# Optimization experiments

Measured on AMD Instinct MI355X. Metric: run time of the kernel, lower is better.

## Reference

```python
import math
import jax, jax.numpy as jnp
import numpy as np

N_NODES = 100000
N_EDGES = 1600000
IN_DIM, HID_DIM, OUT_DIM = 8, 64, 112


def _glorot(key, fan_in, fan_out):
    lim = math.sqrt(6.0 / (fan_in + fan_out))
    return jax.random.uniform(key, (fan_in, fan_out), jnp.float32, -lim, lim)


def _layer_params(key, in_d, out_d):
    ks = jax.random.split(key, 8)
    return dict(
        Wq=_glorot(ks[0], in_d, out_d), bq=jnp.zeros((out_d,), jnp.float32),
        Wk=_glorot(ks[1], in_d, out_d), bk=jnp.zeros((out_d,), jnp.float32),
        Wv=_glorot(ks[2], in_d, out_d), bv=jnp.zeros((out_d,), jnp.float32),
        Ws=_glorot(ks[3], in_d, out_d), bs=jnp.zeros((out_d,), jnp.float32),
    )


def setup_inputs() -> dict:
    key = jax.random.key(0)
    kx, ke, k0, k1, k2 = jax.random.split(key, 5)
    inp = {
        'x': jax.random.normal(kx, (N_NODES, IN_DIM), jnp.float32),
        'edge_index': jax.random.randint(ke, (2, N_EDGES), 0, N_NODES, jnp.int64),
    }
    for li, (kk, ind, outd) in enumerate([(k0, IN_DIM, HID_DIM), (k1, HID_DIM, HID_DIM), (k2, HID_DIM, OUT_DIM)]):
        p = _layer_params(kk, ind, outd)
        for name, v in p.items():
            inp[f'{name}{li}'] = v
    return inp


def _transformer_conv(x, src, dst, Wq, bq, Wk, bk, Wv, bv, Ws, bs):
    # heads=1, concat=True, no edge_attr, eval mode (no dropout)
    N = x.shape[0]
    C = Wq.shape[1]
    q = x @ Wq + bq            # [N, C]
    k = x @ Wk + bk
    v = x @ Wv + bv
    # per-edge attention score: <q_dst, k_src> / sqrt(C)
    scores = jnp.sum(q[dst] * k[src], axis=-1) * (1.0 / math.sqrt(C))  # [E]
    # segment softmax over destination neighborhoods (stable)
    m = jax.ops.segment_max(scores, dst, num_segments=N)               # [N]
    e = jnp.exp(scores - m[dst])                                       # [E]
    denom = jax.ops.segment_sum(e, dst, num_segments=N)                # [N]
    alpha = e / denom[dst]                                             # [E]
    # weighted scatter-add of source values to destinations
    out = jax.ops.segment_sum(alpha[:, None] * v[src], dst, num_segments=N)  # [N, C]
    # root/skip connection
    return out + (x @ Ws + bs)


def reference(x, edge_index,
              Wq0, bq0, Wk0, bk0, Wv0, bv0, Ws0, bs0,
              Wq1, bq1, Wk1, bk1, Wv1, bv1, Ws1, bs1,
              Wq2, bq2, Wk2, bk2, Wv2, bv2, Ws2, bs2):
    src, dst = edge_index[0], edge_index[1]
    h = _transformer_conv(x, src, dst, Wq0, bq0, Wk0, bk0, Wv0, bv0, Ws0, bs0)
    h = jax.nn.relu(h)
    h = _transformer_conv(h, src, dst, Wq1, bq1, Wk1, bk1, Wv1, bv1, Ws1, bs1)
    h = jax.nn.relu(h)
    out = _transformer_conv(h, src, dst, Wq2, bq2, Wk2, bk2, Wv2, bv2, Ws2, bs2)
    return out
```

## Files before the change

### kernel.cpp

```cpp
#include <hip/hip_runtime.h>
#include <hip/hip_fp16.h>
#include <math.h>
#include <float.h>

#define NN 100000
#define NE 1600000

#define SCAN_T 256
#define SCAN_E 1024
#define SCAN_NB ((NN + SCAN_E - 1) / SCAN_E)

#define NBUCK ((NN + 255) / 256)
#define EPB   4096
#define NBLK  ((NE + EPB - 1) / EPB)
#define HISTN (NBUCK * NBLK)
#define GS_NB ((HISTN + SCAN_E - 1) / SCAN_E)
#define BCAP  5120

template<int IN, int OUT, int NPT, int NWIN>
__global__ __launch_bounds__(256)
void linear_qkvs(const float* __restrict__ x,
                 const float* __restrict__ Wq, const float* __restrict__ bq,
                 const float* __restrict__ Wk, const float* __restrict__ bk,
                 const float* __restrict__ Wv, const float* __restrict__ bv,
                 const float* __restrict__ Ws, const float* __restrict__ bs,
                 float* __restrict__ q, unsigned short* __restrict__ kv,
                 float* __restrict__ outskip) {
    const int t    = threadIdx.x;
    const int lane = t & 63;
    const int wv   = t >> 6;
    const int wid  = blockIdx.y * 4 + wv;
    const int mat  = wid / NWIN;
    const int win  = wid % NWIN;
    const int c    = win * 64 + lane;
    const bool act = (c < OUT);
    const int cl   = act ? c : (OUT - 1);

    const float* W = (mat == 0) ? Wq : (mat == 1) ? Wk : (mat == 2) ? Wv : Ws;
    const float* B = (mat == 0) ? bq : (mat == 1) ? bk : (mat == 2) ? bv : bs;

    const int node0 = blockIdx.x * NPT;
    const float* xrow = x + (size_t)node0 * IN;

    float acc[NPT];
    float bias = B[cl];
#pragma unroll
    for (int p = 0; p < NPT; ++p) acc[p] = bias;

    for (int i0 = 0; i0 < IN; i0 += 4) {
        float w0 = W[(size_t)(i0 + 0) * OUT + cl];
        float w1 = W[(size_t)(i0 + 1) * OUT + cl];
        float w2 = W[(size_t)(i0 + 2) * OUT + cl];
        float w3 = W[(size_t)(i0 + 3) * OUT + cl];
#pragma unroll
        for (int p = 0; p < NPT; ++p) {
            float4 xv = *(const float4*)(xrow + p * IN + i0);
            acc[p] += xv.x * w0 + xv.y * w1 + xv.z * w2 + xv.w * w3;
        }
    }

    if (mat == 0) {
        if (act) {
#pragma unroll
            for (int p = 0; p < NPT; ++p)
                q[(size_t)(node0 + p) * OUT + c] = acc[p];
        }
    } else if (mat == 3) {
        if (act) {
#pragma unroll
            for (int p = 0; p < NPT; ++p)
                outskip[(size_t)(node0 + p) * OUT + c] = acc[p];
        }
    } else {
        const int base = (mat == 1) ? 0 : OUT;
#pragma unroll
        for (int p = 0; p < NPT; ++p) {
            float other = __shfl_xor(acc[p], 1);
            if (act && !(lane & 1)) {
                unsigned lo  = __half_as_ushort(__float2half_rn(acc[p]));
                unsigned hiu = __half_as_ushort(__float2half_rn(other));
                *(unsigned*)(kv + (size_t)(node0 + p) * (2 * OUT) + base + c)
                    = lo | (hiu << 16);
            }
        }
    }
}

__global__ __launch_bounds__(256)
void bin_count(const int* __restrict__ ei, int* __restrict__ hist) {
    __shared__ int h[NBUCK];
    const int t = threadIdx.x;
    for (int i = t; i < NBUCK; i += 256) h[i] = 0;
    __syncthreads();
    int e0 = blockIdx.x * EPB;
    int e1 = e0 + EPB < NE ? e0 + EPB : NE;
    for (int i = e0 + t; i < e1; i += 256)
        atomicAdd(&h[ei[NE + i] >> 8], 1);
    __syncthreads();
    for (int i = t; i < NBUCK; i += 256)
        hist[(size_t)i * NBLK + blockIdx.x] = h[i];
}

__global__ __launch_bounds__(SCAN_T)
void gscan1(int* __restrict__ a, int* __restrict__ bsums) {
    __shared__ int lds[SCAN_T];
    int t = threadIdx.x;
    int base = blockIdx.x * SCAN_E + t * 4;
    int vals[4];
    int s = 0;
#pragma unroll
    for (int j = 0; j < 4; ++j) {
        int idx = base + j;
        vals[j] = (idx < HISTN) ? a[idx] : 0;
        s += vals[j];
    }
    lds[t] = s;
    __syncthreads();
    for (int off = 1; off < SCAN_T; off <<= 1) {
        int xx = (t >= off) ? lds[t - off] : 0;
        __syncthreads();
        lds[t] += xx;
        __syncthreads();
    }
    int run = (t > 0) ? lds[t - 1] : 0;
    if (t == SCAN_T - 1) bsums[blockIdx.x] = lds[t];
#pragma unroll
    for (int j = 0; j < 4; ++j) {
        int idx = base + j;
        if (idx < HISTN) a[idx] = run;
        run += vals[j];
    }
}

__global__ __launch_bounds__(256)
void gscan2(int* __restrict__ bsums) {
    __shared__ int lds[256];
    int t = threadIdx.x;
    lds[t] = (t < GS_NB) ? bsums[t] : 0;
    __syncthreads();
    for (int off = 1; off < 256; off <<= 1) {
        int xx = (t >= off) ? lds[t - off] : 0;
        __syncthreads();
        lds[t] += xx;
        __syncthreads();
    }
    if (t < GS_NB) bsums[t] = (t > 0) ? lds[t - 1] : 0;
}

__global__ __launch_bounds__(256)
void gscan3(int* __restrict__ a, const int* __restrict__ bsums,
            int* __restrict__ bstart) {
    int i = blockIdx.x * 256 + threadIdx.x;
    if (i < HISTN) {
        int v = a[i] + bsums[i / SCAN_E];
        a[i] = v;
        if (i % NBLK == 0) bstart[i / NBLK] = v;
    }
    if (i == 0) bstart[NBUCK] = NE;
}

__global__ __launch_bounds__(256)
void bin_scatter(const int* __restrict__ ei, const int* __restrict__ hist,
                 unsigned* __restrict__ ebuf) {
    __shared__ int off[NBUCK];
    const int t = threadIdx.x;
    for (int i = t; i < NBUCK; i += 256)
        off[i] = hist[(size_t)i * NBLK + blockIdx.x];
    __syncthreads();
    int e0 = blockIdx.x * EPB;
    int e1 = e0 + EPB < NE ? e0 + EPB : NE;
    for (int i = e0 + t; i < e1; i += 256) {
        int src = ei[i];
        int dst = ei[NE + i];
        int b = dst >> 8;
        int p = atomicAdd(&off[b], 1);
        ebuf[p] = ((unsigned)(dst & 255) << 17) | (unsigned)src;
    }
}

__global__ __launch_bounds__(256)
void bucket_hist(const int* __restrict__ bstart,
                 const unsigned* __restrict__ ebuf,
                 int* __restrict__ counts) {
    __shared__ int h[256];
    const int b = blockIdx.x;
    const int t = threadIdx.x;
    h[t] = 0;
    __syncthreads();
    int beg = bstart[b], end = bstart[b + 1];
    for (int i = beg + t; i < end; i += 256)
        atomicAdd(&h[ebuf[i] >> 17], 1);
    __syncthreads();
    int d = b * 256 + t;
    if (d < NN) counts[d] = h[t];
}

__global__ __launch_bounds__(SCAN_T)
void scan1(const int* __restrict__ counts, int* __restrict__ offsets,
           int* __restrict__ blocksums) {
    __shared__ int lds[SCAN_T];
    int t = threadIdx.x;
    int base = blockIdx.x * SCAN_E + t * 4;
    int vals[4];
    int s = 0;
#pragma unroll
    for (int j = 0; j < 4; ++j) {
        int idx = base + j;
        vals[j] = (idx < NN) ? counts[idx] : 0;
        s += vals[j];
    }
    lds[t] = s;
    __syncthreads();
    for (int off = 1; off < SCAN_T; off <<= 1) {
        int xx = (t >= off) ? lds[t - off] : 0;
        __syncthreads();
        lds[t] += xx;
        __syncthreads();
    }
    int run = (t > 0) ? lds[t - 1] : 0;
    if (t == SCAN_T - 1) blocksums[blockIdx.x] = lds[t];
#pragma unroll
    for (int j = 0; j < 4; ++j) {
        int idx = base + j;
        if (idx < NN) offsets[idx] = run;
        run += vals[j];
    }
}

__global__ __launch_bounds__(128)
void scan2(int* __restrict__ blocksums) {
    __shared__ int lds[128];
    int t = threadIdx.x;
    lds[t] = (t < SCAN_NB) ? blocksums[t] : 0;
    __syncthreads();
    for (int off = 1; off < 128; off <<= 1) {
        int xx = (t >= off) ? lds[t - off] : 0;
        __syncthreads();
        lds[t] += xx;
        __syncthreads();
    }
    if (t < SCAN_NB) blocksums[t] = (t > 0) ? lds[t - 1] : 0;
}

__global__ __launch_bounds__(256)
void scan3(int* __restrict__ offsets, const int* __restrict__ blocksums) {
    int i = blockIdx.x * blockDim.x + threadIdx.x;
    if (i < NN) offsets[i] = offsets[i] + blocksums[i / SCAN_E];
    if (i == 0) offsets[NN] = NE;
}

__global__ __launch_bounds__(256)
void csr_write(const int* __restrict__ bstart,
               const unsigned* __restrict__ ebuf,
               const int* __restrict__ offsets,
               int* __restrict__ sorted_src) {
    __shared__ int h[256];
    __shared__ int pre[256];
    __shared__ int posi[256];
    __shared__ unsigned srt[BCAP];
    const int b = blockIdx.x;
    const int t = threadIdx.x;
    h[t] = 0;
    __syncthreads();
    int beg = bstart[b];
    int cnt = bstart[b + 1] - beg;
    cnt = cnt < BCAP ? cnt : BCAP;
    const unsigned* buf = ebuf + beg;
    for (int i = t; i < cnt; i += 256)
        atomicAdd(&h[buf[i] >> 17], 1);
    __syncthreads();
    int v = h[t];
    pre[t] = v;
    __syncthreads();
    for (int off = 1; off < 256; off <<= 1) {
        int xx = (t >= off) ? pre[t - off] : 0;
        __syncthreads();
        pre[t] += xx;
        __syncthreads();
    }
    posi[t] = pre[t] - v;
    __syncthreads();
    for (int i = t; i < cnt; i += 256) {
        unsigned u = buf[i];
        int dl = u >> 17;
        int p = atomicAdd(&posi[dl], 1);
        srt[p] = u & 0x1FFFFu;
    }
    __syncthreads();
    const int base = offsets[b << 8];
    for (int i = t; i < cnt; i += 256)
        sorted_src[base + i] = (int)srt[i];
}

__device__ __forceinline__ float row16_sum(float x) {
    int y;
    y = __builtin_amdgcn_update_dpp(0, __float_as_int(x), 0x121, 0xF, 0xF, true); x += __int_as_float(y);
    y = __builtin_amdgcn_update_dpp(0, __float_as_int(x), 0x122, 0xF, 0xF, true); x += __int_as_float(y);
    y = __builtin_amdgcn_update_dpp(0, __float_as_int(x), 0x124, 0xF, 0xF, true); x += __int_as_float(y);
    y = __builtin_amdgcn_update_dpp(0, __float_as_int(x), 0x128, 0xF, 0xF, true); x += __int_as_float(y);
    return x;
}

__device__ __forceinline__ float4 h4_to_f4(uint2 w) {
    union { unsigned u; __half2 h; } a, b;
    a.u = w.x; b.u = w.y;
    float2 f0 = __half22float2(a.h);
    float2 f1 = __half22float2(b.h);
    return make_float4(f0.x, f0.y, f1.x, f1.y);
}

template<int C, bool RELU>
__global__ __launch_bounds__(256)
void attn_gather(const int* __restrict__ offsets,
                 const int* __restrict__ sorted_src,
                 const float* __restrict__ q,
                 const unsigned short* __restrict__ kv,
                 float* __restrict__ out, float scale) {
    const int wid  = (int)((blockIdx.x * blockDim.x + threadIdx.x) >> 6);
    const int lane = threadIdx.x & 63;
    if (wid >= NN) return;
    const int grp = lane >> 4;
    const int ch  = (lane & 15) * 4;
    constexpr bool P2 = (C > 64);
    const bool hi = P2 && (ch + 64 < C);

    const int beg = offsets[wid], end = offsets[wid + 1];

    float4 qv0 = *(const float4*)(q + (size_t)wid * C + ch);
    float4 qv1 = make_float4(0.f, 0.f, 0.f, 0.f);
    if (hi) qv1 = *(const float4*)(q + (size_t)wid * C + ch + 64);

    float m = -FLT_MAX, l = 0.f;
    float4 a0 = make_float4(0.f, 0.f, 0.f, 0.f);
    float4 a1 = make_float4(0.f, 0.f, 0.f, 0.f);

    int i = beg + grp;
    uint2 kw0 = make_uint2(0, 0), vw0 = kw0, kw1 = kw0, vw1 = kw0;
    if (i < end) {
        const unsigned short* row = kv + (size_t)sorted_src[i] * (2 * C);
        kw0 = *(const uint2*)(row + ch);
        vw0 = *(const uint2*)(row + C + ch);
        if (hi) {
            kw1 = *(const uint2*)(row + 64 + ch);
            vw1 = *(const uint2*)(row + C + 64 + ch);
        }
    }
    while (i < end) {
        int inext = i + 4;
        uint2 nkw0 = make_uint2(0, 0), nvw0 = nkw0, nkw1 = nkw0, nvw1 = nkw0;
        if (inext < end) {
            const unsigned short* row = kv + (size_t)sorted_src[inext] * (2 * C);
            nkw0 = *(const uint2*)(row + ch);
            nvw0 = *(const uint2*)(row + C + ch);
            if (hi) {
                nkw1 = *(const uint2*)(row + 64 + ch);
                nvw1 = *(const uint2*)(row + C + 64 + ch);
            }
        }
        float4 kf0 = h4_to_f4(kw0);
        float4 vf0 = h4_to_f4(vw0);
        float part = qv0.x * kf0.x + qv0.y * kf0.y + qv0.z * kf0.z + qv0.w * kf0.w;
        float4 kf1, vf1;
        if (P2) {
            kf1 = h4_to_f4(kw1);
            vf1 = h4_to_f4(vw1);
            part += qv1.x * kf1.x + qv1.y * kf1.y + qv1.z * kf1.z + qv1.w * kf1.w;
        }
        float s = row16_sum(part) * scale;
        float mn = fmaxf(m, s);
        float al = __expf(m - mn);
        float w  = __expf(s - mn);
        l = l * al + w;
        a0.x = a0.x * al + w * vf0.x; a0.y = a0.y * al + w * vf0.y;
        a0.z = a0.z * al + w * vf0.z; a0.w = a0.w * al + w * vf0.w;
        if (P2) {
            a1.x = a1.x * al + w * vf1.x; a1.y = a1.y * al + w * vf1.y;
            a1.z = a1.z * al + w * vf1.z; a1.w = a1.w * al + w * vf1.w;
        }
        m = mn;
        kw0 = nkw0; vw0 = nvw0; kw1 = nkw1; vw1 = nvw1;
        i = inext;
    }

#pragma unroll
    for (int d = 16; d <= 32; d <<= 1) {
        float mo = __shfl_xor(m, d);
        float lo = __shfl_xor(l, d);
        float4 ao0, ao1;
        ao0.x = __shfl_xor(a0.x, d); ao0.y = __shfl_xor(a0.y, d);
        ao0.z = __shfl_xor(a0.z, d); ao0.w = __shfl_xor(a0.w, d);
        if (P2) {
            ao1.x = __shfl_xor(a1.x, d); ao1.y = __shfl_xor(a1.y, d);
            ao1.z = __shfl_xor(a1.z, d); ao1.w = __shfl_xor(a1.w, d);
        }
        float mn = fmaxf(m, mo);
        float e1 = (l  > 0.f) ? __expf(m  - mn) : 0.f;
        float e2 = (lo > 0.f) ? __expf(mo - mn) : 0.f;
        l = l * e1 + lo * e2;
        a0.x = a0.x * e1 + ao0.x * e2; a0.y = a0.y * e1 + ao0.y * e2;
        a0.z = a0.z * e1 + ao0.z * e2; a0.w = a0.w * e1 + ao0.w * e2;
        if (P2) {
            a1.x = a1.x * e1 + ao1.x * e2; a1.y = a1.y * e1 + ao1.y * e2;
            a1.z = a1.z * e1 + ao1.z * e2; a1.w = a1.w * e1 + ao1.w * e2;
        }
        m = mn;
    }

    if (lane < 16) {
        float inv = (l > 0.f) ? 1.f / l : 0.f;
        size_t o = (size_t)wid * C + ch;
        float4 sk = *(const float4*)(out + o);
        float4 r;
        r.x = sk.x + a0.x * inv; r.y = sk.y + a0.y * inv;
        r.z = sk.z + a0.z * inv; r.w = sk.w + a0.w * inv;
        if (RELU) {
            r.x = fmaxf(r.x, 0.f); r.y = fmaxf(r.y, 0.f);
            r.z = fmaxf(r.z, 0.f); r.w = fmaxf(r.w, 0.f);
        }
        *(float4*)(out + o) = r;
        if (hi) {
            float4 sk1 = *(const float4*)(out + o + 64);
            float4 r1;
            r1.x = sk1.x + a1.x * inv; r1.y = sk1.y + a1.y * inv;
            r1.z = sk1.z + a1.z * inv; r1.w = sk1.w + a1.w * inv;
            if (RELU) {
                r1.x = fmaxf(r1.x, 0.f); r1.y = fmaxf(r1.y, 0.f);
                r1.z = fmaxf(r1.z, 0.f); r1.w = fmaxf(r1.w, 0.f);
            }
            *(float4*)(out + o + 64) = r1;
        }
    }
}

template<int IN, int OUT, bool RELU>
static void run_layer(const float* xin, const float* const* Wb,
                      const int* offsets, const int* sorted_src,
                      float* q, unsigned short* kv,
                      float* out, hipStream_t stream) {
    constexpr int NPT  = 16;
    constexpr int NWIN = (OUT + 63) / 64;
    dim3 gl(NN / NPT, NWIN);
    linear_qkvs<IN, OUT, NPT, NWIN><<<gl, 256, 0, stream>>>(
        xin, Wb[0], Wb[1], Wb[2], Wb[3], Wb[4], Wb[5], Wb[6], Wb[7],
        q, kv, out);

    float scale = 1.0f / sqrtf((float)OUT);
    attn_gather<OUT, RELU><<<(NN + 3) / 4, 256, 0, stream>>>(
        offsets, sorted_src, q, kv, out, scale);
}

extern "C" void kernel_launch(void* const* d_in, const int* in_sizes, int n_in,
                              void* d_out, int out_size, void* d_ws, size_t ws_size,
                              hipStream_t stream) {
    const float* x  = (const float*)d_in[0];
    const int*   ei = (const int*)d_in[1];
    const float* Wb0[8], *Wb1[8], *Wb2[8];
    for (int i = 0; i < 8; ++i) {
        Wb0[i] = (const float*)d_in[2 + i];
        Wb1[i] = (const float*)d_in[10 + i];
        Wb2[i] = (const float*)d_in[18 + i];
    }
    float* out = (float*)d_out;

    char* ws = (char*)d_ws;
    const size_t CMAX = 112;
    size_t off = 0;
    float*          q  = (float*)(ws + off);          off += (size_t)NN * CMAX * 4;
    unsigned short* kv = (unsigned short*)(ws + off); off += (size_t)NN * 2 * CMAX * 2;
    float* h0          = (float*)(ws + off);          off += (size_t)NN * 64 * 4;
    float* h1          = (float*)(ws + off);          off += (size_t)NN * 64 * 4;
    int*   sorted_src  = (int*)(ws + off);            off += (size_t)NE * 4;
    int*   counts      = (int*)(ws + off);            off += (size_t)NN * 4;
    int*   offsets     = (int*)(ws + off);            off += (size_t)(NN + 1) * 4;
    int*   blocksums   = (int*)(ws + off);            off += (size_t)SCAN_NB * 4;
    int*   hist        = (int*)(ws + off);            off += (size_t)HISTN * 4;
    int*   gsums       = (int*)(ws + off);            off += (size_t)GS_NB * 4;
    int*   bstart      = (int*)(ws + off);            off += (size_t)(NBUCK + 1) * 4;
    unsigned* ebuf     = (unsigned*)(ws + off);       off += (size_t)NE * 4;
    (void)ws_size; (void)in_sizes; (void)n_in; (void)out_size;

    bin_count<<<NBLK, 256, 0, stream>>>(ei, hist);
    gscan1<<<GS_NB, SCAN_T, 0, stream>>>(hist, gsums);
    gscan2<<<1, 256, 0, stream>>>(gsums);
    gscan3<<<(HISTN + 255) / 256, 256, 0, stream>>>(hist, gsums, bstart);
    bin_scatter<<<NBLK, 256, 0, stream>>>(ei, hist, ebuf);
    bucket_hist<<<NBUCK, 256, 0, stream>>>(bstart, ebuf, counts);
    scan1<<<SCAN_NB, SCAN_T, 0, stream>>>(counts, offsets, blocksums);
    scan2<<<1, 128, 0, stream>>>(blocksums);
    scan3<<<(NN + 255) / 256, 256, 0, stream>>>(offsets, blocksums);
    csr_write<<<NBUCK, 256, 0, stream>>>(bstart, ebuf, offsets, sorted_src);

    run_layer<8,  64, true >(x,  Wb0, offsets, sorted_src, q, kv, h0,  stream);
    run_layer<64, 64, true >(h0, Wb1, offsets, sorted_src, q, kv, h1,  stream);
    run_layer<64, 112, false>(h1, Wb2, offsets, sorted_src, q, kv, out, stream);
}
```

Before: 631.2 us.

## Compute QKVS projections with split-bf16 MFMA instead of scalar FP32 FMA

Replaces the scalar FP32 linear kernel with an MFMA-based GEMM that splits both activations and weights into bf16 hi/lo parts and accumulates three 16x16x32 products to keep close to FP32 accuracy. A new prep kernel repacks the weights into the MFMA fragment layout once per call, placed in the workspace after the edge buffer once CSR building is done. The goal is to cut the per-layer projection cost, paid for with extra conversion work, three MFMAs per tile and a small precision loss from dropping the lo*lo term.

```diff
diff --git a/kernel.cpp b/kernel.cpp
--- a/kernel.cpp
+++ b/kernel.cpp
@@ -2,6 +2,7 @@
 #include <hip/hip_fp16.h>
 #include <math.h>
 #include <float.h>
+#include <stdint.h>
 
 #define NN 100000
 #define NE 1600000
@@ -17,70 +18,153 @@
 #define GS_NB ((HISTN + SCAN_E - 1) / SCAN_E)
 #define BCAP  5120
 
-template<int IN, int OUT, int NPT, int NWIN>
-__global__ __launch_bounds__(256)
-void linear_qkvs(const float* __restrict__ x,
-                 const float* __restrict__ Wq, const float* __restrict__ bq,
-                 const float* __restrict__ Wk, const float* __restrict__ bk,
-                 const float* __restrict__ Wv, const float* __restrict__ bv,
-                 const float* __restrict__ Ws, const float* __restrict__ bs,
-                 float* __restrict__ q, unsigned short* __restrict__ kv,
-                 float* __restrict__ outskip) {
+typedef __attribute__((ext_vector_type(8))) short short8v;
+typedef __attribute__((ext_vector_type(4))) float float4v;
+
+__device__ __forceinline__ unsigned short f32_to_bf16_rne(float f) {
+    unsigned u = __float_as_uint(f);
+    u += 0x7FFFu + ((u >> 16) & 1u);
+    return (unsigned short)(u >> 16);
+}
+__device__ __forceinline__ float bf16_to_f32(unsigned short h) {
+    return __uint_as_float(((unsigned)h) << 16);
+}
+
+template<int K, int OUT>
+__global__ __launch_bounds__(256)
+void prep_w(const float* __restrict__ Wq, const float* __restrict__ Wk,
+            const float* __restrict__ Wv, const float* __restrict__ Ws,
+            unsigned short* __restrict__ wsp) {
+    constexpr int NKS  = (K + 31) / 32;
+    constexpr int OUTT = 4 * OUT;
+    constexpr int NCT  = OUTT / 16;
+    int idx = blockIdx.x * 256 + threadIdx.x;
+    if (idx >= NCT * NKS * 512) return;
+    int j    = idx & 7;
+    int lane = (idx >> 3) & 63;
+    int cell = idx >> 9;
+    int ks   = cell % NKS;
+    int ct   = cell / NKS;
+    int g = lane >> 4, ln = lane & 15;
+    int k = ks * 32 + g * 8 + j;
+    int c = ct * 16 + ln;
+    int mat = c / OUT, cm = c % OUT;
+    const float* W = (mat == 0) ? Wq : (mat == 1) ? Wk : (mat == 2) ? Wv : Ws;
+    float f = (k < K) ? W[(size_t)k * OUT + cm] : 0.f;
+    unsigned short h = f32_to_bf16_rne(f);
+    float resid = f - bf16_to_f32(h);
+    wsp[(size_t)cell * 1024 + lane * 8 + j]       = h;
+    wsp[(size_t)cell * 1024 + 512 + lane * 8 + j] = f32_to_bf16_rne(resid);
+}
+
+template<int K, int OUT, int CTSPLIT>
+__global__ __launch_bounds__(256)
+void gemm_qkvs(const float* __restrict__ x,
+               const unsigned short* __restrict__ wsp,
+               const float* __restrict__ bq, const float* __restrict__ bk,
+               const float* __restrict__ bv, const float* __restrict__ bs,
+               float* __restrict__ q, unsigned short* __restrict__ kv,
+               float* __restrict__ outskip) {
+    constexpr int NKS  = (K + 31) / 32;
+    constexpr int OUTT = 4 * OUT;
+    constexpr int NCT  = OUTT / 16;
+    constexpr int CTPB = NCT / CTSPLIT;
+
     const int t    = threadIdx.x;
     const int lane = t & 63;
     const int wv   = t >> 6;
-    const int wid  = blockIdx.y * 4 + wv;
-    const int mat  = wid / NWIN;
-    const int win  = wid % NWIN;
-    const int c    = win * 64 + lane;
-    const bool act = (c < OUT);
-    const int cl   = act ? c : (OUT - 1);
-
-    const float* W = (mat == 0) ? Wq : (mat == 1) ? Wk : (mat == 2) ? Wv : Ws;
-    const float* B = (mat == 0) ? bq : (mat == 1) ? bk : (mat == 2) ? bv : bs;
-
-    const int node0 = blockIdx.x * NPT;
-    const float* xrow = x + (size_t)node0 * IN;
-
-    float acc[NPT];
-    float bias = B[cl];
-#pragma unroll
-    for (int p = 0; p < NPT; ++p) acc[p] = bias;
-
-    for (int i0 = 0; i0 < IN; i0 += 4) {
-        float w0 = W[(size_t)(i0 + 0) * OUT + cl];
-        float w1 = W[(size_t)(i0 + 1) * OUT + cl];
-        float w2 = W[(size_t)(i0 + 2) * OUT + cl];
-        float w3 = W[(size_t)(i0 + 3) * OUT + cl];
-#pragma unroll
-        for (int p = 0; p < NPT; ++p) {
-            float4 xv = *(const float4*)(xrow + p * IN + i0);
-            acc[p] += xv.x * w0 + xv.y * w1 + xv.z * w2 + xv.w * w3;
-        }
-    }
-
-    if (mat == 0) {
-        if (act) {
-#pragma unroll
-            for (int p = 0; p < NPT; ++p)
-                q[(size_t)(node0 + p) * OUT + c] = acc[p];
-        }
-    } else if (mat == 3) {
-        if (act) {
-#pragma unroll
-            for (int p = 0; p < NPT; ++p)
-                outskip[(size_t)(node0 + p) * OUT + c] = acc[p];
-        }
-    } else {
-        const int base = (mat == 1) ? 0 : OUT;
-#pragma unroll
-        for (int p = 0; p < NPT; ++p) {
-            float other = __shfl_xor(acc[p], 1);
-            if (act && !(lane & 1)) {
-                unsigned lo  = __half_as_ushort(__float2half_rn(acc[p]));
-                unsigned hiu = __half_as_ushort(__float2half_rn(other));
-                *(unsigned*)(kv + (size_t)(node0 + p) * (2 * OUT) + base + c)
-                    = lo | (hiu << 16);
+    const int g    = lane >> 4;
+    const int ln   = lane & 15;
+    const int rowbase = (blockIdx.x * 4 + wv) * 32;
+    if (rowbase >= NN) return;
+
+    union F8 { short8v v; unsigned short s[8]; uint4 u4; };
+
+    F8 ahi[2][NKS], alo[2][NKS];
+#pragma unroll
+    for (int rt = 0; rt < 2; ++rt) {
+        int r = rowbase + rt * 16 + ln;
+        if (r >= NN) r = NN - 1;
+        const float* rowp = x + (size_t)r * K;
+#pragma unroll
+        for (int ks = 0; ks < NKS; ++ks) {
+            const int k0 = ks * 32 + g * 8;
+            float xv[8];
+            if (k0 + 8 <= K) {
+                float4 p0 = *(const float4*)(rowp + k0);
+                float4 p1 = *(const float4*)(rowp + k0 + 4);
+                xv[0] = p0.x; xv[1] = p0.y; xv[2] = p0.z; xv[3] = p0.w;
+                xv[4] = p1.x; xv[5] = p1.y; xv[6] = p1.z; xv[7] = p1.w;
+            } else {
+#pragma unroll
+                for (int j = 0; j < 8; ++j) xv[j] = 0.f;
+            }
+#pragma unroll
+            for (int j = 0; j < 8; ++j) {
+                unsigned short h = f32_to_bf16_rne(xv[j]);
+                ahi[rt][ks].s[j] = h;
+                alo[rt][ks].s[j] = f32_to_bf16_rne(xv[j] - bf16_to_f32(h));
+            }
+        }
+    }
+
+    const int ct0 = blockIdx.y * CTPB;
+#pragma unroll 1
+    for (int ct = ct0; ct < ct0 + CTPB; ++ct) {
+        F8 bhi[NKS], blo[NKS];
+        const unsigned short* wp = wsp + (size_t)(ct * NKS) * 1024 + lane * 8;
+#pragma unroll
+        for (int ks = 0; ks < NKS; ++ks) {
+            bhi[ks].u4 = *(const uint4*)(wp + ks * 1024);
+            blo[ks].u4 = *(const uint4*)(wp + ks * 1024 + 512);
+        }
+
+        const int cb  = ct * 16;
+        const int mat = cb / OUT;
+        const int cm  = (cb % OUT) + ln;
+        const float* B = (mat == 0) ? bq : (mat == 1) ? bk : (mat == 2) ? bv : bs;
+        const float bias = B[cm];
+        float4v acc0 = {bias, bias, bias, bias};
+        float4v acc1 = {bias, bias, bias, bias};
+#pragma unroll
+        for (int ks = 0; ks < NKS; ++ks) {
+            acc0 = __builtin_amdgcn_mfma_f32_16x16x32_bf16(ahi[0][ks].v, blo[ks].v, acc0, 0, 0, 0);
+            acc0 = __builtin_amdgcn_mfma_f32_16x16x32_bf16(alo[0][ks].v, bhi[ks].v, acc0, 0, 0, 0);
+            acc0 = __builtin_amdgcn_mfma_f32_16x16x32_bf16(ahi[0][ks].v, bhi[ks].v, acc0, 0, 0, 0);
+            acc1 = __builtin_amdgcn_mfma_f32_16x16x32_bf16(ahi[1][ks].v, blo[ks].v, acc1, 0, 0, 0);
+            acc1 = __builtin_amdgcn_mfma_f32_16x16x32_bf16(alo[1][ks].v, bhi[ks].v, acc1, 0, 0, 0);
+            acc1 = __builtin_amdgcn_mfma_f32_16x16x32_bf16(ahi[1][ks].v, bhi[ks].v, acc1, 0, 0, 0);
+        }
+
+        if (mat == 0 || mat == 3) {
+            float* dst = (mat == 0) ? q : outskip;
+#pragma unroll
+            for (int rt = 0; rt < 2; ++rt) {
+                float4v a = rt ? acc1 : acc0;
+#pragma unroll
+                for (int reg = 0; reg < 4; ++reg) {
+                    int node = rowbase + rt * 16 + g * 4 + reg;
+                    if (node < NN)
+                        dst[(size_t)node * OUT + cm] = a[reg];
+                }
+            }
+        } else {
+            const int base = (mat == 1) ? 0 : OUT;
+#pragma unroll
+            for (int rt = 0; rt < 2; ++rt) {
+                float4v a = rt ? acc1 : acc0;
+#pragma unroll
+                for (int reg = 0; reg < 4; ++reg) {
+                    int node = rowbase + rt * 16 + g * 4 + reg;
+                    float f = a[reg];
+                    float other = __shfl_xor(f, 1);
+                    if (node < NN && !(ln & 1)) {
+                        unsigned lo16 = __half_as_ushort(__float2half_rn(f));
+                        unsigned hi16 = __half_as_ushort(__float2half_rn(other));
+                        *(unsigned*)(kv + (size_t)node * (2 * OUT) + base + cm)
+                            = lo16 | (hi16 << 16);
+                    }
+                }
             }
         }
     }
@@ -432,17 +516,16 @@
     }
 }
 
-template<int IN, int OUT, bool RELU>
-static void run_layer(const float* xin, const float* const* Wb,
+template<int K, int OUT, bool RELU>
+static void run_layer(const float* xin, const unsigned short* wsp,
+                      const float* const* Wb,
                       const int* offsets, const int* sorted_src,
                       float* q, unsigned short* kv,
                       float* out, hipStream_t stream) {
-    constexpr int NPT  = 16;
-    constexpr int NWIN = (OUT + 63) / 64;
-    dim3 gl(NN / NPT, NWIN);
-    linear_qkvs<IN, OUT, NPT, NWIN><<<gl, 256, 0, stream>>>(
-        xin, Wb[0], Wb[1], Wb[2], Wb[3], Wb[4], Wb[5], Wb[6], Wb[7],
-        q, kv, out);
+    constexpr int CTSPLIT = 2;
+    dim3 gg((NN + 127) / 128, CTSPLIT);
+    gemm_qkvs<K, OUT, CTSPLIT><<<gg, 256, 0, stream>>>(
+        xin, wsp, Wb[1], Wb[3], Wb[5], Wb[7], q, kv, out);
 
     float scale = 1.0f / sqrtf((float)OUT);
     attn_gather<OUT, RELU><<<(NN + 3) / 4, 256, 0, stream>>>(
@@ -490,7 +573,19 @@
     scan3<<<(NN + 255) / 256, 256, 0, stream>>>(offsets, blocksums);
     csr_write<<<NBUCK, 256, 0, stream>>>(bstart, ebuf, offsets, sorted_src);
 
-    run_layer<8,  64, true >(x,  Wb0, offsets, sorted_src, q, kv, h0,  stream);
-    run_layer<64, 64, true >(h0, Wb1, offsets, sorted_src, q, kv, h1,  stream);
-    run_layer<64, 112, false>(h1, Wb2, offsets, sorted_src, q, kv, out, stream);
-}
+    unsigned short* wspbase =
+        (unsigned short*)(((uintptr_t)ebuf + 255) & ~(uintptr_t)255);
+    unsigned short* wsp0 = wspbase;
+    unsigned short* wsp1 = wsp0 + 16 * 1 * 1024;
+    unsigned short* wsp2 = wsp1 + 16 * 2 * 1024;
+    prep_w<8, 64><<<(16 * 1 * 512 + 255) / 256, 256, 0, stream>>>(
+        Wb0[0], Wb0[2], Wb0[4], Wb0[6], wsp0);
+    prep_w<64, 64><<<(16 * 2 * 512 + 255) / 256, 256, 0, stream>>>(
+        Wb1[0], Wb1[2], Wb1[4], Wb1[6], wsp1);
+    prep_w<64, 112><<<(28 * 2 * 512 + 255) / 256, 256, 0, stream>>>(
+        Wb2[0], Wb2[2], Wb2[4], Wb2[6], wsp2);
+
+    run_layer<8,  64, true >(x,  wsp0, Wb0, offsets, sorted_src, q, kv, h0,  stream);
+    run_layer<64, 64, true >(h0, wsp1, Wb1, offsets, sorted_src, q, kv, h1,  stream);
+    run_layer<64, 112, false>(h1, wsp2, Wb2, offsets, sorted_src, q, kv, out, stream);
+}
```

After: 555.7 us. -12.0%, faster.
